# Performance work log

Measured on AMD Instinct MI355X. Metric: run time of the kernel, lower is better.

## Reference

```python
import jax, jax.numpy as jnp
import numpy as np

N_NODES = 50000
N_EDGES = 800000
IN_DIM = 128
HID = 128
N_GRAPHS = 64


def setup_inputs() -> dict:
    key = jax.random.key(0)
    ks = jax.random.split(key, 12)
    edge_index = jax.random.randint(ks[0], (2, N_EDGES), 0, N_NODES, dtype=jnp.int64)
    edge_weight = jax.random.uniform(ks[1], (N_EDGES,), dtype=jnp.float32)
    input_feature = jax.random.normal(ks[2], (N_NODES, IN_DIM), dtype=jnp.float32)
    graph_indicator = jnp.sort(jax.random.randint(ks[3], (N_NODES,), 0, N_GRAPHS, dtype=jnp.int64))
    s = 0.05
    W1 = jax.random.normal(ks[4], (IN_DIM, HID), dtype=jnp.float32) * s
    b1 = jnp.zeros((HID,), jnp.float32)
    W2 = jax.random.normal(ks[5], (HID, HID), dtype=jnp.float32) * s
    b2 = jnp.zeros((HID,), jnp.float32)
    W3 = jax.random.normal(ks[6], (HID, HID), dtype=jnp.float32) * s
    b3 = jnp.zeros((HID,), jnp.float32)
    wa = jax.random.normal(ks[7], (3 * HID, 1), dtype=jnp.float32) * s
    ba = jnp.zeros((1,), jnp.float32)
    Wf = jax.random.normal(ks[8], (3 * HID * 2, IN_DIM), dtype=jnp.float32) * s
    bf = jnp.zeros((IN_DIM,), jnp.float32)
    return dict(edge_index=edge_index, edge_weight=edge_weight,
                input_feature=input_feature, graph_indicator=graph_indicator,
                W1=W1, b1=b1, W2=W2, b2=b2, W3=W3, b3=b3,
                wa=wa, ba=ba, Wf=Wf, bf=bf)


def reference(edge_index, edge_weight, input_feature, graph_indicator,
              W1, b1, W2, b2, W3, b3, wa, ba, Wf, bf):
    src, dst = edge_index[0], edge_index[1]

    def gcn(x, W, b):
        # GraphConvolution: adj @ (x @ W) + b, adj given as weighted edge list
        support = x @ W  # [N, d_out]
        msg = edge_weight[:, None] * support[src]  # [E, d_out] gather
        return jax.ops.segment_sum(msg, dst, num_segments=N_NODES) + b

    g1 = jax.nn.relu(gcn(input_feature, W1, b1))
    g2 = jax.nn.relu(gcn(g1, W2, b2))
    g3 = jax.nn.relu(gcn(g2, W3, b3))
    h = jnp.concatenate([g1, g2, g3], axis=1)  # [N, 3*HID]

    # SelfAttentionPooling: attention score via a 1-dim GraphConvolution, tanh gate
    score = jnp.tanh(gcn(h, wa, ba))  # [N, 1]
    pool = h * score

    # segment avg / max pooling per graph
    seg_sum = jax.ops.segment_sum(pool, graph_indicator, num_segments=N_GRAPHS)
    counts = jax.ops.segment_sum(jnp.ones((N_NODES, 1), pool.dtype), graph_indicator,
                                 num_segments=N_GRAPHS)
    avg = seg_sum / jnp.maximum(counts, 1.0)
    mx = jax.ops.segment_max(pool, graph_indicator, num_segments=N_GRAPHS)
    pooled = jnp.concatenate([avg, mx], axis=1)  # [G, 6*HID]

    return jax.nn.relu(pooled @ Wf + bf)  # [G, IN_DIM]
```

## Files before the change

kernel.cpp:

```cpp
#include <hip/hip_runtime.h>
#include <math.h>

#define HID 128
#define POOL_SEG 16
#define WT_STRIDE 136
#define ELL_D 48
#define SC_CHUNK 2048
#define FXS 16384.0f
#define FXI (1.0f/16384.0f)

typedef __attribute__((ext_vector_type(8))) short short8;
typedef __attribute__((ext_vector_type(4))) float float4v;

__device__ inline short f2bf(float f) {
  unsigned u = __builtin_bit_cast(unsigned, f);
  unsigned r = (u + 0x7fff + ((u >> 16) & 1)) >> 16;
  return (short)r;
}
__device__ inline unsigned pack2bf(float lo, float hi) {
  return (unsigned)(unsigned short)f2bf(lo) | ((unsigned)(unsigned short)f2bf(hi) << 16);
}
__device__ inline float bflo(unsigned u) { return __builtin_bit_cast(float, u << 16); }
__device__ inline float bfhi(unsigned u) { return __builtin_bit_cast(float, u & 0xffff0000u); }
__device__ inline float bf2f(unsigned short s) { return __builtin_bit_cast(float, (unsigned)s << 16); }
__device__ inline unsigned short f2h(float f) {
  _Float16 h = (_Float16)f;
  return __builtin_bit_cast(unsigned short, h);
}
__device__ inline float h2f(unsigned short hb) {
  return (float)__builtin_bit_cast(_Float16, hb);
}

__global__ __launch_bounds__(256) void prologue(
    const void* __restrict__ ei_raw, const float* __restrict__ ew,
    int2* __restrict__ packed, int* __restrict__ cursor, int* __restrict__ s_pre_fx,
    const float* __restrict__ W1, const float* __restrict__ W2, const float* __restrict__ W3,
    short* __restrict__ T1, short* __restrict__ T2, short* __restrict__ T3,
    const void* __restrict__ gi_raw, int* __restrict__ gstart,
    int E, int N, int G, int EB) {
  int b = blockIdx.x, t = threadIdx.x;
  if (b < EB) {
    int gid = b * 256 + t;
    if (gid < N) { cursor[gid] = 0; s_pre_fx[gid] = 0; }
    if (gid < E) {
      const int* pw = (const int*)ei_raw;
      int nz = 0;
#pragma unroll
      for (int i = 1; i < 64; i += 2) nz |= pw[i];
      int s, d;
      if (nz == 0) {
        const long long* p = (const long long*)ei_raw;
        s = (int)p[gid]; d = (int)p[E + gid];
      } else {
        const int* p = (const int*)ei_raw;
        s = p[gid]; d = p[E + gid];
      }
      packed[gid] = make_int2((d << 16) | s, __builtin_bit_cast(int, ew[gid]));
    }
  } else if (b < EB + 192) {
    int i = (b - EB) * 256 + t;
    int which = i >> 14, idx = i & 16383;
    int k = idx >> 7, nn = idx & 127;
    const float* W = (which == 0) ? W1 : ((which == 1) ? W2 : W3);
    short* T = (which == 0) ? T1 : ((which == 1) ? T2 : T3);
    T[nn * WT_STRIDE + k] = f2bf(W[idx]);
  } else {
    int g = t;
    if (g > G) return;
    if (g == G) { gstart[g] = N; return; }
    bool is64 = (((const int*)gi_raw)[N - 1] == 0);
    const long long* g64 = (const long long*)gi_raw;
    const int* g32 = (const int*)gi_raw;
    int lo = 0, hi = N;
    while (lo < hi) {
      int mid = (lo + hi) >> 1;
      long long v = is64 ? g64[mid] : (long long)g32[mid];
      if (v < (long long)g) lo = mid + 1; else hi = mid;
    }
    gstart[g] = lo;
  }
}

__global__ void scatter_ell(const int2* __restrict__ packed, int* __restrict__ cursor,
                            unsigned* __restrict__ ell, int E, int N) {
  int group = blockIdx.x & 7;
  int chunk = blockIdx.x >> 3;
  int rng = (N + 7) >> 3;
  int lo = group * rng;
  int hi = lo + rng; if (hi > N) hi = N;
  int base = chunk * SC_CHUNK;
  for (int i = 0; i < SC_CHUNK; i += 256) {
    int e = base + i + threadIdx.x;
    if (e < E) {
      int2 rec = packed[e];
      int d = ((unsigned)rec.x) >> 16;
      if (d >= lo && d < hi) {
        unsigned s = (unsigned)rec.x & 0xFFFFu;
        unsigned short wh = f2h(__builtin_bit_cast(float, rec.y));
        int pos = atomicAdd(&cursor[d], 1);
        if (pos < ELL_D)
          ell[(size_t)d * ELL_D + pos] = (s << 16) | (unsigned)wh;
      }
    }
  }
}

__global__ __launch_bounds__(256) void gemm_mfma(const float* __restrict__ Af,
                                                 const unsigned short* __restrict__ Abf,
                                                 const short* __restrict__ Wt,
                                                 unsigned short* __restrict__ C,
                                                 int n, int a_is_bf16) {
  __shared__ short Wlds[128 * WT_STRIDE];
  int t = threadIdx.x;
  {
    const ulonglong2* gsrc = (const ulonglong2*)Wt;
    ulonglong2* ldst = (ulonglong2*)Wlds;
    for (int i = t; i < (128 * WT_STRIDE) / 8; i += 256) ldst[i] = gsrc[i];
  }
  __syncthreads();

  int wave = t >> 6, lane = t & 63;
  int quad = lane >> 4, l15 = lane & 15;
  int m0 = blockIdx.x * 64 + wave * 16;
  size_t SL = (size_t)n * 32;

  int m = m0 + l15; if (m >= n) m = n - 1;
  short8 afrag[4];
  if (a_is_bf16) {
#pragma unroll
    for (int c = 0; c < 4; c++)
      afrag[c] = *(const short8*)(Abf + c * SL + (size_t)m * 32 + quad * 8);
  } else {
    const float* Arow = Af + (size_t)m * 128;
#pragma unroll
    for (int c = 0; c < 4; c++) {
      int k0 = c * 32 + quad * 8;
      float4 x = *(const float4*)(Arow + k0);
      float4 y = *(const float4*)(Arow + k0 + 4);
      short8 a;
      a[0] = f2bf(x.x); a[1] = f2bf(x.y); a[2] = f2bf(x.z); a[3] = f2bf(x.w);
      a[4] = f2bf(y.x); a[5] = f2bf(y.y); a[6] = f2bf(y.z); a[7] = f2bf(y.w);
      afrag[c] = a;
    }
  }

  float4v acc[8];
#pragma unroll
  for (int tt = 0; tt < 8; tt++) acc[tt] = (float4v){0.f, 0.f, 0.f, 0.f};

#pragma unroll
  for (int c = 0; c < 4; c++) {
    int kb = c * 32 + quad * 8;
#pragma unroll
    for (int tt = 0; tt < 8; tt++) {
      const short8* bp = (const short8*)&Wlds[(tt * 16 + l15) * WT_STRIDE + kb];
      acc[tt] = __builtin_amdgcn_mfma_f32_16x16x32_bf16(afrag[c], *bp, acc[tt], 0, 0, 0);
    }
  }

  int rbase = m0 + quad * 4;
#pragma unroll
  for (int tt = 0; tt < 8; tt++) {
    int within = (tt & 1) * 16 + l15;
    size_t sb = (size_t)(tt >> 1) * SL;
#pragma unroll
    for (int r = 0; r < 4; r++) {
      int row = rbase + r;
      if (row < n) C[sb + (size_t)row * 32 + within] = (unsigned short)f2bf(acc[tt][r]);
    }
  }
}

__global__ __launch_bounds__(256) void aggregate_sl(
    const unsigned short* __restrict__ support, const int* __restrict__ deg_arr,
    const unsigned* __restrict__ ell, const float* __restrict__ bias,
    unsigned short* __restrict__ out,
    const unsigned short* __restrict__ g1p, const unsigned short* __restrict__ g2p,
    const float* __restrict__ wa, int* __restrict__ s_pre_fx,
    int n, int halfN, int do_score) {
  int g = blockIdx.x & 7;
  int chunk = blockIdx.x >> 3;
  int slice = g >> 1, half = g & 1;
  int t = threadIdx.x;
  int local = chunk * 64 + (t >> 2);
  int q = t & 3;
  if (local >= halfN) return;
  int node = half * halfN + local;
  if (node >= n) return;

  int deg = deg_arr[node]; if (deg > ELL_D) deg = ELL_D;
  const unsigned* row = ell + (size_t)node * ELL_D;
  const uint4* sb = (const uint4*)support + (size_t)slice * n * 4 + q;

  int acc[8];
#pragma unroll
  for (int j = 0; j < 8; j++) acc[j] = 0;

  int i = 0;
  for (; i + 3 < deg; i += 4) {
    uint4 rr = *(const uint4*)(row + i);
    float w0 = h2f((unsigned short)(rr.x & 0xFFFF)) * FXS;
    float w1 = h2f((unsigned short)(rr.y & 0xFFFF)) * FXS;
    float w2 = h2f((unsigned short)(rr.z & 0xFFFF)) * FXS;
    float w3 = h2f((unsigned short)(rr.w & 0xFFFF)) * FXS;
    uint4 v0 = sb[(size_t)(rr.x >> 16) * 4];
    uint4 v1 = sb[(size_t)(rr.y >> 16) * 4];
    uint4 v2 = sb[(size_t)(rr.z >> 16) * 4];
    uint4 v3 = sb[(size_t)(rr.w >> 16) * 4];
    acc[0] += __float2int_rn(w0 * bflo(v0.x)); acc[1] += __float2int_rn(w0 * bfhi(v0.x));
    acc[2] += __float2int_rn(w0 * bflo(v0.y)); acc[3] += __float2int_rn(w0 * bfhi(v0.y));
    acc[4] += __float2int_rn(w0 * bflo(v0.z)); acc[5] += __float2int_rn(w0 * bfhi(v0.z));
    acc[6] += __float2int_rn(w0 * bflo(v0.w)); acc[7] += __float2int_rn(w0 * bfhi(v0.w));
    acc[0] += __float2int_rn(w1 * bflo(v1.x)); acc[1] += __float2int_rn(w1 * bfhi(v1.x));
    acc[2] += __float2int_rn(w1 * bflo(v1.y)); acc[3] += __float2int_rn(w1 * bfhi(v1.y));
    acc[4] += __float2int_rn(w1 * bflo(v1.z)); acc[5] += __float2int_rn(w1 * bfhi(v1.z));
    acc[6] += __float2int_rn(w1 * bflo(v1.w)); acc[7] += __float2int_rn(w1 * bfhi(v1.w));
    acc[0] += __float2int_rn(w2 * bflo(v2.x)); acc[1] += __float2int_rn(w2 * bfhi(v2.x));
    acc[2] += __float2int_rn(w2 * bflo(v2.y)); acc[3] += __float2int_rn(w2 * bfhi(v2.y));
    acc[4] += __float2int_rn(w2 * bflo(v2.z)); acc[5] += __float2int_rn(w2 * bfhi(v2.z));
    acc[6] += __float2int_rn(w2 * bflo(v2.w)); acc[7] += __float2int_rn(w2 * bfhi(v2.w));
    acc[0] += __float2int_rn(w3 * bflo(v3.x)); acc[1] += __float2int_rn(w3 * bfhi(v3.x));
    acc[2] += __float2int_rn(w3 * bflo(v3.y)); acc[3] += __float2int_rn(w3 * bfhi(v3.y));
    acc[4] += __float2int_rn(w3 * bflo(v3.z)); acc[5] += __float2int_rn(w3 * bfhi(v3.z));
    acc[6] += __float2int_rn(w3 * bflo(v3.w)); acc[7] += __float2int_rn(w3 * bfhi(v3.w));
  }
  for (; i < deg; i++) {
    unsigned r0 = row[i];
    float w0 = h2f((unsigned short)(r0 & 0xFFFF)) * FXS;
    uint4 v0 = sb[(size_t)(r0 >> 16) * 4];
    acc[0] += __float2int_rn(w0 * bflo(v0.x)); acc[1] += __float2int_rn(w0 * bfhi(v0.x));
    acc[2] += __float2int_rn(w0 * bflo(v0.y)); acc[3] += __float2int_rn(w0 * bfhi(v0.y));
    acc[4] += __float2int_rn(w0 * bflo(v0.z)); acc[5] += __float2int_rn(w0 * bfhi(v0.z));
    acc[6] += __float2int_rn(w0 * bflo(v0.w)); acc[7] += __float2int_rn(w0 * bfhi(v0.w));
  }

  float f[8];
#pragma unroll
  for (int j = 0; j < 8; j++) f[j] = (float)acc[j] * FXI;

  float4 b0 = ((const float4*)bias)[slice * 8 + q * 2];
  float4 b1 = ((const float4*)bias)[slice * 8 + q * 2 + 1];
  f[0] = fmaxf(f[0] + b0.x, 0.f); f[1] = fmaxf(f[1] + b0.y, 0.f);
  f[2] = fmaxf(f[2] + b0.z, 0.f); f[3] = fmaxf(f[3] + b0.w, 0.f);
  f[4] = fmaxf(f[4] + b1.x, 0.f); f[5] = fmaxf(f[5] + b1.y, 0.f);
  f[6] = fmaxf(f[6] + b1.z, 0.f); f[7] = fmaxf(f[7] + b1.w, 0.f);

  uint4 o;
  o.x = pack2bf(f[0], f[1]); o.y = pack2bf(f[2], f[3]);
  o.z = pack2bf(f[4], f[5]); o.w = pack2bf(f[6], f[7]);
  ((uint4*)out)[(size_t)slice * n * 4 + (size_t)node * 4 + q] = o;

  if (do_score) {
    uint4 u1 = ((const uint4*)g1p)[(size_t)slice * n * 4 + (size_t)node * 4 + q];
    uint4 u2 = ((const uint4*)g2p)[(size_t)slice * n * 4 + (size_t)node * 4 + q];
    const float* wa1 = wa + slice * 32 + q * 8;
    const float* wa2 = wa1 + 128;
    const float* wa3 = wa1 + 256;
    float sc = bflo(u1.x) * wa1[0] + bfhi(u1.x) * wa1[1]
             + bflo(u1.y) * wa1[2] + bfhi(u1.y) * wa1[3]
             + bflo(u1.z) * wa1[4] + bfhi(u1.z) * wa1[5]
             + bflo(u1.w) * wa1[6] + bfhi(u1.w) * wa1[7]
             + bflo(u2.x) * wa2[0] + bfhi(u2.x) * wa2[1]
             + bflo(u2.y) * wa2[2] + bfhi(u2.y) * wa2[3]
             + bflo(u2.z) * wa2[4] + bfhi(u2.z) * wa2[5]
             + bflo(u2.w) * wa2[6] + bfhi(u2.w) * wa2[7];
#pragma unroll
    for (int j = 0; j < 8; j++) sc += f[j] * wa3[j];
    sc += __shfl_xor(sc, 1, 64);
    sc += __shfl_xor(sc, 2, 64);
    if (q == 0) atomicAdd(&s_pre_fx[node], __float2int_rn(sc * FXS));
  }
}

__global__ void att_aggregate(const int* __restrict__ s_pre_fx, const int* __restrict__ deg_arr,
                              const unsigned* __restrict__ ell,
                              const float* __restrict__ ba, float* __restrict__ score, int n) {
  int node = blockIdx.x * blockDim.x + threadIdx.x;
  if (node >= n) return;
  int deg = deg_arr[node]; if (deg > ELL_D) deg = ELL_D;
  const unsigned* row = ell + (size_t)node * ELL_D;
  int acc = 0;
  for (int i = 0; i < deg; i++) {
    unsigned r = row[i];
    acc += __float2int_rn(h2f((unsigned short)(r & 0xFFFF)) * (float)s_pre_fx[r >> 16]);
  }
  score[node] = tanhf((float)acc * FXI + ba[0]);
}

__global__ __launch_bounds__(384) void pool_partial(const unsigned short* __restrict__ g1,
                                                    const unsigned short* __restrict__ g2,
                                                    const unsigned short* __restrict__ g3,
                                                    const float* __restrict__ score,
                                                    const int* __restrict__ gstart,
                                                    float* __restrict__ part, int n) {
  int g = blockIdx.x / POOL_SEG, seg = blockIdx.x % POOL_SEG;
  int d = threadIdx.x;
  int sg = d >> 7, dd = d & 127;
  const unsigned short* gp = (sg == 0) ? g1 : ((sg == 1) ? g2 : g3);
  const unsigned short* col = gp + (size_t)(dd >> 5) * ((size_t)n * 32) + (dd & 31);
  int s = gstart[g], e = gstart[g + 1];
  int len = e - s;
  int chunk = (len + POOL_SEG - 1) / POOL_SEG;
  int ns = s + seg * chunk;
  int ne = ns + chunk; if (ne > e) ne = e;
  float sum = 0.f, mx = -3.402823466e38f;
  for (int node = ns; node < ne; node++) {
    float sc = score[node];
    float v = bf2f(col[(size_t)node * 32]) * sc;
    sum += v;
    mx = fmaxf(mx, v);
  }
  size_t base = (size_t)blockIdx.x * 768;
  part[base + d] = sum;
  part[base + 384 + d] = mx;
}

__global__ __launch_bounds__(512) void tail(const float* __restrict__ part,
                                            const int* __restrict__ gstart,
                                            const float* __restrict__ Wf,
                                            const float* __restrict__ bfb,
                                            float* __restrict__ out) {
  __shared__ float pooled[768];
  __shared__ float red[512];
  int g = blockIdx.x, t = threadIdx.x;
  float cnt = (float)(gstart[g + 1] - gstart[g]);
  float inv = 1.0f / fmaxf(cnt, 1.0f);
  if (t < 384) {
    int d = t;
    float sum = 0.f, mx = -3.402823466e38f;
    for (int seg = 0; seg < POOL_SEG; seg++) {
      size_t base = ((size_t)g * POOL_SEG + seg) * 768;
      sum += part[base + d];
      mx = fmaxf(mx, part[base + 384 + d]);
    }
    pooled[d] = sum * inv;
    pooled[384 + d] = mx;
  }
  __syncthreads();
  int kc = t >> 7, c = t & 127;
  float acc = (kc == 0) ? bfb[c] : 0.f;
  int k0 = kc * 192;
#pragma unroll 8
  for (int k = k0; k < k0 + 192; k++) acc += pooled[k] * Wf[(size_t)k * 128 + c];
  red[t] = acc;
  __syncthreads();
  if (t < 128)
    out[(size_t)g * 128 + t] =
        fmaxf(red[t] + red[t + 128] + red[t + 256] + red[t + 384], 0.f);
}

extern "C" void kernel_launch(void* const* d_in, const int* in_sizes, int n_in,
                              void* d_out, int out_size, void* d_ws, size_t ws_size,
                              hipStream_t stream) {
  const void* ei_raw = d_in[0];
  const float* ew    = (const float*)d_in[1];
  const float* X     = (const float*)d_in[2];
  const void* gi_raw = d_in[3];
  const float* W1 = (const float*)d_in[4];  const float* b1 = (const float*)d_in[5];
  const float* W2 = (const float*)d_in[6];  const float* b2 = (const float*)d_in[7];
  const float* W3 = (const float*)d_in[8];  const float* b3 = (const float*)d_in[9];
  const float* wa = (const float*)d_in[10]; const float* ba = (const float*)d_in[11];
  const float* Wf = (const float*)d_in[12]; const float* bf = (const float*)d_in[13];
  float* out = (float*)d_out;

  const int E = in_sizes[1];
  const int N = in_sizes[2] / 128;
  const int G = out_size / 128;

  char* ws = (char*)d_ws;
  size_t off = 0;
  auto take = [&](size_t bytes) {
    char* p = ws + off;
    off = (off + bytes + 255) & ~(size_t)255;
    return p;
  };
  int*      cursor  = (int*)take((size_t)N * 4);
  int2*     packed  = (int2*)take((size_t)E * 8);
  unsigned* ell     = (unsigned*)take((size_t)N * ELL_D * 4);
  short*    wt1     = (short*)take((size_t)128 * WT_STRIDE * 2);
  short*    wt2     = (short*)take((size_t)128 * WT_STRIDE * 2);
  short*    wt3     = (short*)take((size_t)128 * WT_STRIDE * 2);
  unsigned short* support = (unsigned short*)take((size_t)N * 128 * 2);
  unsigned short* g1      = (unsigned short*)take((size_t)N * 128 * 2);
  unsigned short* g2      = (unsigned short*)take((size_t)N * 128 * 2);
  unsigned short* g3      = (unsigned short*)take((size_t)N * 128 * 2);
  int*   s_pre_fx = (int*)take((size_t)N * 4);
  float* score    = (float*)take((size_t)N * 4);
  int*   gstart   = (int*)take((size_t)(G + 1) * 4);
  float* part     = (float*)take((size_t)G * POOL_SEG * 768 * 4);
  if (off > ws_size) return;

  const int EB = (E + 255) / 256;
  prologue<<<EB + 192 + 1, 256, 0, stream>>>(ei_raw, ew, packed, cursor, s_pre_fx,
                                             W1, W2, W3, wt1, wt2, wt3,
                                             gi_raw, gstart, E, N, G, EB);
  {
    int chunks = (E + SC_CHUNK - 1) / SC_CHUNK;
    scatter_ell<<<8 * chunks, 256, 0, stream>>>(packed, cursor, ell, E, N);
  }

  const int GB = (N + 63) / 64;
  const int halfN = (N + 1) / 2;
  const int AGB = 8 * ((halfN + 63) / 64);
  gemm_mfma<<<GB, 256, 0, stream>>>(X, (const unsigned short*)nullptr, wt1, support, N, 0);
  aggregate_sl<<<AGB, 256, 0, stream>>>(support, cursor, ell, b1, g1,
                                        nullptr, nullptr, nullptr, nullptr, N, halfN, 0);
  gemm_mfma<<<GB, 256, 0, stream>>>((const float*)nullptr, g1, wt2, support, N, 1);
  aggregate_sl<<<AGB, 256, 0, stream>>>(support, cursor, ell, b2, g2,
                                        nullptr, nullptr, nullptr, nullptr, N, halfN, 0);
  gemm_mfma<<<GB, 256, 0, stream>>>((const float*)nullptr, g2, wt3, support, N, 1);
  aggregate_sl<<<AGB, 256, 0, stream>>>(support, cursor, ell, b3, g3,
                                        g1, g2, wa, s_pre_fx, N, halfN, 1);

  att_aggregate<<<(N + 255) / 256, 256, 0, stream>>>(s_pre_fx, cursor, ell, ba, score, N);

  pool_partial<<<G * POOL_SEG, 384, 0, stream>>>(g1, g2, g3, score, gstart, part, N);
  tail<<<G, 512, 0, stream>>>(part, gstart, Wf, bf, out);
}
```

Before: 326.5 us.

## Fuse ELL build into prologue, degree-sort aggregation nodes, fold attention into pooling

The prologue now builds the ELL adjacency directly with per-destination atomics, which removes the packed edge buffer and the separate range-filtered scatter kernel. A degree histogram, a scan and a permutation (built by extra blocks appended to the first GEMM launch) order the nodes by degree, so the aggregation waves get uniform trip counts. The attention-score aggregation is fused into pool_partial through a shared-memory tile, and zeroing moves to a single memset. In exchange it adds atomic contention on the prologue scatter, extra small kernels, and less locality in the permuted node order.

```diff
diff --git a/kernel.cpp b/kernel.cpp
--- a/kernel.cpp
+++ b/kernel.cpp
@@ -5,7 +5,6 @@
 #define POOL_SEG 16
 #define WT_STRIDE 136
 #define ELL_D 48
-#define SC_CHUNK 2048
 #define FXS 16384.0f
 #define FXI (1.0f/16384.0f)
 
@@ -33,16 +32,15 @@
 
 __global__ __launch_bounds__(256) void prologue(
     const void* __restrict__ ei_raw, const float* __restrict__ ew,
-    int2* __restrict__ packed, int* __restrict__ cursor, int* __restrict__ s_pre_fx,
+    int* __restrict__ cursor, unsigned* __restrict__ ell,
     const float* __restrict__ W1, const float* __restrict__ W2, const float* __restrict__ W3,
     short* __restrict__ T1, short* __restrict__ T2, short* __restrict__ T3,
     const void* __restrict__ gi_raw, int* __restrict__ gstart,
     int E, int N, int G, int EB) {
   int b = blockIdx.x, t = threadIdx.x;
   if (b < EB) {
-    int gid = b * 256 + t;
-    if (gid < N) { cursor[gid] = 0; s_pre_fx[gid] = 0; }
-    if (gid < E) {
+    int e = b * 256 + t;
+    if (e < E) {
       const int* pw = (const int*)ei_raw;
       int nz = 0;
 #pragma unroll
@@ -50,12 +48,15 @@
       int s, d;
       if (nz == 0) {
         const long long* p = (const long long*)ei_raw;
-        s = (int)p[gid]; d = (int)p[E + gid];
+        s = (int)p[e]; d = (int)p[E + e];
       } else {
         const int* p = (const int*)ei_raw;
-        s = p[gid]; d = p[E + gid];
+        s = p[e]; d = p[E + e];
       }
-      packed[gid] = make_int2((d << 16) | s, __builtin_bit_cast(int, ew[gid]));
+      unsigned short wh = f2h(ew[e]);
+      int pos = atomicAdd(&cursor[d], 1);
+      if (pos < ELL_D)
+        ell[(size_t)d * ELL_D + pos] = ((unsigned)s << 16) | (unsigned)wh;
     }
   } else if (b < EB + 192) {
     int i = (b - EB) * 256 + t;
@@ -81,27 +82,25 @@
   }
 }
 
-__global__ void scatter_ell(const int2* __restrict__ packed, int* __restrict__ cursor,
-                            unsigned* __restrict__ ell, int E, int N) {
-  int group = blockIdx.x & 7;
-  int chunk = blockIdx.x >> 3;
-  int rng = (N + 7) >> 3;
-  int lo = group * rng;
-  int hi = lo + rng; if (hi > N) hi = N;
-  int base = chunk * SC_CHUNK;
-  for (int i = 0; i < SC_CHUNK; i += 256) {
-    int e = base + i + threadIdx.x;
-    if (e < E) {
-      int2 rec = packed[e];
-      int d = ((unsigned)rec.x) >> 16;
-      if (d >= lo && d < hi) {
-        unsigned s = (unsigned)rec.x & 0xFFFFu;
-        unsigned short wh = f2h(__builtin_bit_cast(float, rec.y));
-        int pos = atomicAdd(&cursor[d], 1);
-        if (pos < ELL_D)
-          ell[(size_t)d * ELL_D + pos] = (s << 16) | (unsigned)wh;
-      }
-    }
+__global__ __launch_bounds__(256) void hist_k(const int* __restrict__ cursor,
+                                              int* __restrict__ hist, int n) {
+  __shared__ int lh[ELL_D + 1];
+  int t = threadIdx.x;
+  if (t <= ELL_D) lh[t] = 0;
+  __syncthreads();
+  int i = blockIdx.x * 256 + t;
+  if (i < n) {
+    int d = cursor[i]; if (d > ELL_D) d = ELL_D;
+    atomicAdd(&lh[d], 1);
+  }
+  __syncthreads();
+  if (t <= ELL_D && lh[t]) atomicAdd(&hist[t], lh[t]);
+}
+
+__global__ void scan_k(const int* __restrict__ hist, int* __restrict__ bbase) {
+  if (threadIdx.x == 0) {
+    int r = 0;
+    for (int d = 0; d <= ELL_D; d++) { bbase[d] = r; r += hist[d]; }
   }
 }
 
@@ -109,7 +108,20 @@
                                                  const unsigned short* __restrict__ Abf,
                                                  const short* __restrict__ Wt,
                                                  unsigned short* __restrict__ C,
-                                                 int n, int a_is_bf16) {
+                                                 int n, int a_is_bf16, int gemm_nb,
+                                                 const int* __restrict__ deg,
+                                                 const int* __restrict__ bbase,
+                                                 int* __restrict__ bcur,
+                                                 int* __restrict__ perm) {
+  if (blockIdx.x >= gemm_nb) {
+    int idx = (blockIdx.x - gemm_nb) * 256 + threadIdx.x;
+    if (idx < n) {
+      int dg = deg[idx]; if (dg > ELL_D) dg = ELL_D;
+      int pos = atomicAdd(&bcur[dg], 1);
+      perm[bbase[dg] + pos] = idx;
+    }
+    return;
+  }
   __shared__ short Wlds[128 * WT_STRIDE];
   int t = threadIdx.x;
   {
@@ -177,16 +189,15 @@
     unsigned short* __restrict__ out,
     const unsigned short* __restrict__ g1p, const unsigned short* __restrict__ g2p,
     const float* __restrict__ wa, int* __restrict__ s_pre_fx,
-    int n, int halfN, int do_score) {
-  int g = blockIdx.x & 7;
-  int chunk = blockIdx.x >> 3;
-  int slice = g >> 1, half = g & 1;
+    const int* __restrict__ perm, int n, int do_score) {
+  int group = blockIdx.x & 7;
+  int slice = group >> 1;
+  int chunk = (blockIdx.x >> 3) * 2 + (group & 1);
   int t = threadIdx.x;
-  int local = chunk * 64 + (t >> 2);
+  int pos = chunk * 64 + (t >> 2);
   int q = t & 3;
-  if (local >= halfN) return;
-  int node = half * halfN + local;
-  if (node >= n) return;
+  if (pos >= n) return;
+  int node = perm[pos];
 
   int deg = deg_arr[node]; if (deg > ELL_D) deg = ELL_D;
   const unsigned* row = ell + (size_t)node * ELL_D;
@@ -272,30 +283,18 @@
   }
 }
 
-__global__ void att_aggregate(const int* __restrict__ s_pre_fx, const int* __restrict__ deg_arr,
-                              const unsigned* __restrict__ ell,
-                              const float* __restrict__ ba, float* __restrict__ score, int n) {
-  int node = blockIdx.x * blockDim.x + threadIdx.x;
-  if (node >= n) return;
-  int deg = deg_arr[node]; if (deg > ELL_D) deg = ELL_D;
-  const unsigned* row = ell + (size_t)node * ELL_D;
-  int acc = 0;
-  for (int i = 0; i < deg; i++) {
-    unsigned r = row[i];
-    acc += __float2int_rn(h2f((unsigned short)(r & 0xFFFF)) * (float)s_pre_fx[r >> 16]);
-  }
-  score[node] = tanhf((float)acc * FXI + ba[0]);
-}
-
 __global__ __launch_bounds__(384) void pool_partial(const unsigned short* __restrict__ g1,
                                                     const unsigned short* __restrict__ g2,
                                                     const unsigned short* __restrict__ g3,
-                                                    const float* __restrict__ score,
+                                                    const int* __restrict__ s_pre_fx,
+                                                    const int* __restrict__ deg_arr,
+                                                    const unsigned* __restrict__ ell,
+                                                    const float* __restrict__ ba,
                                                     const int* __restrict__ gstart,
                                                     float* __restrict__ part, int n) {
   int g = blockIdx.x / POOL_SEG, seg = blockIdx.x % POOL_SEG;
-  int d = threadIdx.x;
-  int sg = d >> 7, dd = d & 127;
+  int t = threadIdx.x;
+  int sg = t >> 7, dd = t & 127;
   const unsigned short* gp = (sg == 0) ? g1 : ((sg == 1) ? g2 : g3);
   const unsigned short* col = gp + (size_t)(dd >> 5) * ((size_t)n * 32) + (dd & 31);
   int s = gstart[g], e = gstart[g + 1];
@@ -303,16 +302,33 @@
   int chunk = (len + POOL_SEG - 1) / POOL_SEG;
   int ns = s + seg * chunk;
   int ne = ns + chunk; if (ne > e) ne = e;
+  float ba0 = ba[0];
+  __shared__ float sc_lds[256];
   float sum = 0.f, mx = -3.402823466e38f;
-  for (int node = ns; node < ne; node++) {
-    float sc = score[node];
-    float v = bf2f(col[(size_t)node * 32]) * sc;
-    sum += v;
-    mx = fmaxf(mx, v);
+  for (int tb = ns; tb < ne; tb += 256) {
+    int te = tb + 256; if (te > ne) te = ne;
+    __syncthreads();
+    if (t < te - tb) {
+      int node = tb + t;
+      int deg = deg_arr[node]; if (deg > ELL_D) deg = ELL_D;
+      const unsigned* row = ell + (size_t)node * ELL_D;
+      int acc = 0;
+      for (int i = 0; i < deg; i++) {
+        unsigned r = row[i];
+        acc += __float2int_rn(h2f((unsigned short)(r & 0xFFFF)) * (float)s_pre_fx[r >> 16]);
+      }
+      sc_lds[t] = tanhf((float)acc * FXI + ba0);
+    }
+    __syncthreads();
+    for (int node = tb; node < te; node++) {
+      float v = bf2f(col[(size_t)node * 32]) * sc_lds[node - tb];
+      sum += v;
+      mx = fmaxf(mx, v);
+    }
   }
   size_t base = (size_t)blockIdx.x * 768;
-  part[base + d] = sum;
-  part[base + 384 + d] = mx;
+  part[base + t] = sum;
+  part[base + 384 + t] = mx;
 }
 
 __global__ __launch_bounds__(512) void tail(const float* __restrict__ part,
@@ -374,46 +390,52 @@
     off = (off + bytes + 255) & ~(size_t)255;
     return p;
   };
-  int*      cursor  = (int*)take((size_t)N * 4);
-  int2*     packed  = (int2*)take((size_t)E * 8);
-  unsigned* ell     = (unsigned*)take((size_t)N * ELL_D * 4);
-  short*    wt1     = (short*)take((size_t)128 * WT_STRIDE * 2);
-  short*    wt2     = (short*)take((size_t)128 * WT_STRIDE * 2);
-  short*    wt3     = (short*)take((size_t)128 * WT_STRIDE * 2);
+  int* zb = (int*)take((size_t)N * 8 + 512);
+  int* cursor   = zb;
+  int* s_pre_fx = zb + N;
+  int* hist     = zb + 2 * N;
+  int* bcur     = zb + 2 * N + 64;
+  int* bbase    = (int*)take(256);
+  int* perm     = (int*)take((size_t)N * 4);
+  unsigned* ell = (unsigned*)take((size_t)N * ELL_D * 4);
+  short*    wt1 = (short*)take((size_t)128 * WT_STRIDE * 2);
+  short*    wt2 = (short*)take((size_t)128 * WT_STRIDE * 2);
+  short*    wt3 = (short*)take((size_t)128 * WT_STRIDE * 2);
   unsigned short* support = (unsigned short*)take((size_t)N * 128 * 2);
   unsigned short* g1      = (unsigned short*)take((size_t)N * 128 * 2);
   unsigned short* g2      = (unsigned short*)take((size_t)N * 128 * 2);
   unsigned short* g3      = (unsigned short*)take((size_t)N * 128 * 2);
-  int*   s_pre_fx = (int*)take((size_t)N * 4);
-  float* score    = (float*)take((size_t)N * 4);
-  int*   gstart   = (int*)take((size_t)(G + 1) * 4);
-  float* part     = (float*)take((size_t)G * POOL_SEG * 768 * 4);
+  int*   gstart  = (int*)take((size_t)(G + 1) * 4);
+  float* part    = (float*)take((size_t)G * POOL_SEG * 768 * 4);
   if (off > ws_size) return;
 
+  hipMemsetAsync(zb, 0, (size_t)N * 8 + 512, stream);
+
   const int EB = (E + 255) / 256;
-  prologue<<<EB + 192 + 1, 256, 0, stream>>>(ei_raw, ew, packed, cursor, s_pre_fx,
+  prologue<<<EB + 192 + 1, 256, 0, stream>>>(ei_raw, ew, cursor, ell,
                                              W1, W2, W3, wt1, wt2, wt3,
                                              gi_raw, gstart, E, N, G, EB);
-  {
-    int chunks = (E + SC_CHUNK - 1) / SC_CHUNK;
-    scatter_ell<<<8 * chunks, 256, 0, stream>>>(packed, cursor, ell, E, N);
-  }
+  const int NB256 = (N + 255) / 256;
+  hist_k<<<NB256, 256, 0, stream>>>(cursor, hist, N);
+  scan_k<<<1, 64, 0, stream>>>(hist, bbase);
 
   const int GB = (N + 63) / 64;
-  const int halfN = (N + 1) / 2;
-  const int AGB = 8 * ((halfN + 63) / 64);
-  gemm_mfma<<<GB, 256, 0, stream>>>(X, (const unsigned short*)nullptr, wt1, support, N, 0);
+  const int NB64 = (N + 63) / 64;
+  const int AGB = 8 * ((NB64 + 1) / 2);
+  gemm_mfma<<<GB + NB256, 256, 0, stream>>>(X, (const unsigned short*)nullptr, wt1,
+                                            support, N, 0, GB, cursor, bbase, bcur, perm);
   aggregate_sl<<<AGB, 256, 0, stream>>>(support, cursor, ell, b1, g1,
-                                        nullptr, nullptr, nullptr, nullptr, N, halfN, 0);
-  gemm_mfma<<<GB, 256, 0, stream>>>((const float*)nullptr, g1, wt2, support, N, 1);
+                                        nullptr, nullptr, nullptr, nullptr, perm, N, 0);
+  gemm_mfma<<<GB, 256, 0, stream>>>((const float*)nullptr, g1, wt2, support, N, 1, GB,
+                                    nullptr, nullptr, nullptr, nullptr);
   aggregate_sl<<<AGB, 256, 0, stream>>>(support, cursor, ell, b2, g2,
-                                        nullptr, nullptr, nullptr, nullptr, N, halfN, 0);
-  gemm_mfma<<<GB, 256, 0, stream>>>((const float*)nullptr, g2, wt3, support, N, 1);
+                                        nullptr, nullptr, nullptr, nullptr, perm, N, 0);
+  gemm_mfma<<<GB, 256, 0, stream>>>((const float*)nullptr, g2, wt3, support, N, 1, GB,
+                                    nullptr, nullptr, nullptr, nullptr);
   aggregate_sl<<<AGB, 256, 0, stream>>>(support, cursor, ell, b3, g3,
-                                        g1, g2, wa, s_pre_fx, N, halfN, 1);
-
-  att_aggregate<<<(N + 255) / 256, 256, 0, stream>>>(s_pre_fx, cursor, ell, ba, score, N);
-
-  pool_partial<<<G * POOL_SEG, 384, 0, stream>>>(g1, g2, g3, score, gstart, part, N);
+                                        g1, g2, wa, s_pre_fx, perm, N, 1);
+
+  pool_partial<<<G * POOL_SEG, 384, 0, stream>>>(g1, g2, g3, s_pre_fx, cursor, ell,
+                                                 ba, gstart, part, N);
   tail<<<G, 512, 0, stream>>>(part, gstart, Wf, bf, out);
 }
```

Result: slower. 459.5 us (+40.7%).
